# Performance work log

Measured on AMD Instinct MI355X. Metric: run time of the kernel, lower is better.

The kernel has to match this reference:

```python
import jax, jax.numpy as jnp
import numpy as np
import math

T, N, D = 512, 128, 64
H, HID, OUT = 4, 64, 64
BLOCK = 512


def setup_inputs() -> dict:
    key = jax.random.key(0)
    ks = jax.random.split(key, 6)
    x = jax.random.normal(ks[0], (T, N, D), dtype=jnp.float32)
    pe_table = jax.random.normal(ks[1], (BLOCK, N * D), dtype=jnp.float32) * 0.02
    wq = jax.random.normal(ks[2], (H, HID, D), dtype=jnp.float32) / math.sqrt(D)
    wk = jax.random.normal(ks[3], (H, HID, D), dtype=jnp.float32) / math.sqrt(D)
    wv = jax.random.normal(ks[4], (H, OUT, D), dtype=jnp.float32) / math.sqrt(D)
    wo = jax.random.normal(ks[5], (OUT, H * HID), dtype=jnp.float32) / math.sqrt(H * HID)
    return {"x": x, "pe_table": pe_table, "wq": wq, "wk": wk, "wv": wv, "wo": wo}


def reference(x, pe_table, wq, wk, wv, wo):
    # x: [T, N, D]. Positional encoding: embedding row per time index t.
    t, n, d = x.shape
    pe = pe_table[:t].reshape(t, n, d)
    xin = x + pe  # dropout is identity in eval mode

    hid = wq.shape[1]
    # nn.Linear(bias=False): y = x @ W.T, W is [out, in]
    Q = jnp.einsum('tnd,hed->htne', xin, wq)  # [H, T, N, HID]
    K = jnp.einsum('tnd,hed->htne', xin, wk)
    V = jnp.einsum('tnd,hod->htno', xin, wv)  # [H, T, N, OUT]

    # per-node attention over time: scores[h,t,n,s] = Q[h,t,n]·K[h,s,n] / sqrt(hid)
    scores = jnp.einsum('htne,hsne->htns', Q, K) / math.sqrt(hid)

    # causal (sequent) mask over (t, s), masked_fill(mask==0, -1e9)
    causal = jnp.tril(jnp.ones((t, t), dtype=bool))  # [T, T]
    scores = jnp.where(causal[None, :, None, :], scores, jnp.float32(-1e9))

    p = jax.nn.softmax(scores, axis=-1)  # [H, T, N, T]
    heads = jnp.einsum('htns,hsno->htno', p, V)  # [H, T, N, OUT]

    # concat heads along feature dim, then output projection
    heads = heads.transpose(1, 2, 0, 3).reshape(t, n, -1)  # [T, N, H*OUT]
    out = heads @ wo.T  # [T, N, OUT]
    return out
```

## Files before the change

kernel.cpp:

```cpp
#include <hip/hip_runtime.h>

using short8 = __attribute__((ext_vector_type(8))) short;
using f32x4  = __attribute__((ext_vector_type(4))) float;
using u16x4  = __attribute__((ext_vector_type(4))) unsigned short;

#define MFMA16(A,B,C) __builtin_amdgcn_mfma_f32_16x16x32_bf16((A),(B),(C),0,0,0)

#if __has_builtin(__builtin_amdgcn_exp2f)
#define EXP2(x) __builtin_amdgcn_exp2f(x)
#else
#define EXP2(x) exp2f(x)
#endif

__device__ __forceinline__ unsigned short f2b(float f) {
  unsigned u = __float_as_uint(f);
  return (unsigned short)((u + 0x7fffu + ((u >> 16) & 1u)) >> 16);
}
__device__ __forceinline__ short8 mk8(unsigned a, unsigned b, unsigned c, unsigned d) {
  union { unsigned u[4]; short8 s; } t; t.u[0]=a; t.u[1]=b; t.u[2]=c; t.u[3]=d; return t.s;
}
__device__ __forceinline__ unsigned pk2(float lo, float hi) {
  return __builtin_amdgcn_perm(__float_as_uint(hi), __float_as_uint(lo), 0x07060302u);
}


__global__ void prep_kernel(const float* __restrict__ x, const float* __restrict__ pe,
                            unsigned* __restrict__ xinT,
                            const float* __restrict__ wq, const float* __restrict__ wk,
                            const float* __restrict__ wv, const float* __restrict__ wo,
                            unsigned short* __restrict__ wP) {
  int b = blockIdx.x;
  if (b >= 8192) {
    int idx = (b - 8192) * 256 + threadIdx.x;
    int a = idx >> 14, e = idx & 16383;
    const float SC = 0.18033688011112042f;
    float v = (a == 0) ? wq[e] * SC : (a == 1) ? wk[e] : (a == 2) ? wv[e] : wo[e];
    wP[idx] = f2b(v);
    return;
  }
  int i2 = b * 256 + threadIdx.x;
  const float2* xp = (const float2*)x;
  const float2* pp = (const float2*)pe;
  float2 a = xp[i2], c = pp[i2];
  float s0 = a.x + c.x, s1 = a.y + c.y;
  int i = i2 << 1;
  int t = i >> 13, rem = i & 8191, n = rem >> 6, d = rem & 63;
  unsigned v = (unsigned)f2b(s0) | ((unsigned)f2b(s1) << 16);
  xinT[((n * 512 + t) * 64 + d) >> 1] = v;
}

__device__ __forceinline__ void qprojT(
    const unsigned short* xn, const unsigned short* bqP, int qb16,
    int lg, int lm, short8 (&qB)[2]) {
  const f32x4 zero4 = {0.f, 0.f, 0.f, 0.f};
  short8 aX0 = *(const short8*)(xn + (qb16 + lm) * 64 + lg * 8);
  short8 aX1 = *(const short8*)(xn + (qb16 + lm) * 64 + 32 + lg * 8);
  f32x4 qt[4];
#pragma unroll
  for (int nt = 0; nt < 4; ++nt) {
    const unsigned short* p = bqP + (nt * 16 + lm) * 64 + lg * 8;
    short8 w0 = *(const short8*)p;
    short8 w1 = *(const short8*)(p + 32);
    f32x4 a = zero4;
    a = MFMA16(w0, aX0, a);
    a = MFMA16(w1, aX1, a);
    qt[nt] = a;
  }
#pragma unroll
  for (int ks = 0; ks < 2; ++ks) {
    short8 q;
#pragma unroll
    for (int i = 0; i < 8; ++i) q[i] = (short)f2b(qt[2 * ks + (i >> 2)][i & 3]);
    qB[ks] = q;
  }
}

__device__ __forceinline__ void stage_slab(
    const unsigned short* xn, int slab, int lg, int lm, int l,
    const unsigned short* bkP, const unsigned short* bvP,
    unsigned short* sK, short8* sVf) {
  const f32x4 zero4 = {0.f, 0.f, 0.f, 0.f};
  int s0 = slab * 32;
  short8 aX[2][2];
#pragma unroll
  for (int km = 0; km < 2; ++km) {
    aX[km][0] = *(const short8*)(xn + (s0 + km * 16 + lm) * 64 + lg * 8);
    aX[km][1] = *(const short8*)(xn + (s0 + km * 16 + lm) * 64 + 32 + lg * 8);
  }
#pragma unroll
  for (int nt = 0; nt < 4; ++nt) {
    const unsigned short* bko = bkP + (nt * 16 + lm) * 64 + lg * 8;
    const unsigned short* bvo = bvP + (nt * 16 + lm) * 64 + lg * 8;
    short8 wk0 = *(const short8*)bko, wk1 = *(const short8*)(bko + 32);
    short8 wv0 = *(const short8*)bvo, wv1 = *(const short8*)(bvo + 32);
    f32x4 k0 = zero4, k1 = zero4, v0 = zero4, v1 = zero4;
    k0 = MFMA16(aX[0][0], wk0, k0); k0 = MFMA16(aX[0][1], wk1, k0);
    k1 = MFMA16(aX[1][0], wk0, k1); k1 = MFMA16(aX[1][1], wk1, k1);
    v0 = MFMA16(aX[0][0], wv0, v0); v0 = MFMA16(aX[0][1], wv1, v0);
    v1 = MFMA16(aX[1][0], wv0, v1); v1 = MFMA16(aX[1][1], wv1, v1);
    int pos = ((nt & 2) << 4) + ((lm >> 2) << 3) + ((nt & 1) << 2) + (lm & 3);
#pragma unroll
    for (int r = 0; r < 4; ++r) {
      int row0 = s0 + lg * 4 + r;
      int row1 = s0 + 16 + lg * 4 + r;
      sK[row0 * 64 + (pos ^ ((row0 & 7) << 3))] = f2b(k0[r]);
      sK[row1 * 64 + (pos ^ ((row1 & 7) << 3))] = f2b(k1[r]);
    }
    short8 vv;
    vv[0]=(short)f2b(v0[0]); vv[1]=(short)f2b(v0[1]);
    vv[2]=(short)f2b(v0[2]); vv[3]=(short)f2b(v0[3]);
    vv[4]=(short)f2b(v1[0]); vv[5]=(short)f2b(v1[1]);
    vv[6]=(short)f2b(v1[2]); vv[7]=(short)f2b(v1[3]);
    sVf[(slab * 4 + nt) * 64 + l] = vv;
  }
}

__device__ __forceinline__ void load_vB(const short8* sVf, int kb, int l, short8 (&vB)[4]) {
#pragma unroll
  for (int ot = 0; ot < 4; ++ot) vB[ot] = sVf[(((kb >> 5) * 4) + ot) * 64 + l];
}

__device__ __forceinline__ void slab_body(
    const unsigned short* sK, const short8 (&vB)[4], const short8 (&qB)[2][2],
    f32x4 (&oAcc)[2][4], f32x4 (&lsAcc)[2], const short8 ones,
    int qb, int kb, int lg, int lm) {
  const f32x4 zero4 = {0.f, 0.f, 0.f, 0.f};
  short8 aK[2][2];
#pragma unroll
  for (int km = 0; km < 2; ++km) {
    int row = kb + km * 16 + lm;
    int rb = row * 64, xorv = (row & 7) << 3;
    aK[km][0] = *(const short8*)&sK[rb + ((lg * 8) ^ xorv)];
    aK[km][1] = *(const short8*)&sK[rb + ((32 + lg * 8) ^ xorv)];
  }
  f32x4 st[2][2];
#pragma unroll
  for (int km = 0; km < 2; ++km)
#pragma unroll
    for (int qn = 0; qn < 2; ++qn) {
      f32x4 a = zero4;
      a = MFMA16(aK[km][0], qB[qn][0], a);
      a = MFMA16(aK[km][1], qB[qn][1], a);
      st[km][qn] = a;
    }
  if (kb == qb) {
#pragma unroll
    for (int km = 0; km < 2; ++km)
#pragma unroll
      for (int qn = 0; qn < 2; ++qn) {
        if (km == 0 && qn == 1) continue;
#pragma unroll
        for (int r = 0; r < 4; ++r) {
          int key = km * 16 + lg * 4 + r, qr = qn * 16 + lm;
          if (key > qr) st[km][qn][r] = -1e30f;
        }
      }
  }
#pragma unroll
  for (int km = 0; km < 2; ++km)
#pragma unroll
    for (int qn = 0; qn < 2; ++qn)
#pragma unroll
      for (int r = 0; r < 4; ++r) st[km][qn][r] = EXP2(st[km][qn][r]);
#pragma unroll
  for (int mo = 0; mo < 2; ++mo) {
    short8 pA = mk8(pk2(st[0][mo][0], st[0][mo][1]), pk2(st[0][mo][2], st[0][mo][3]),
                    pk2(st[1][mo][0], st[1][mo][1]), pk2(st[1][mo][2], st[1][mo][3]));
    lsAcc[mo] = MFMA16(ones, pA, lsAcc[mo]);
#pragma unroll
    for (int ot = 0; ot < 4; ++ot) oAcc[mo][ot] = MFMA16(vB[ot], pA, oAcc[mo][ot]);
  }
}

__global__ __launch_bounds__(512) void attn_kernel(
    const unsigned short* __restrict__ xinT,
    const unsigned short* __restrict__ wP,
    unsigned short* __restrict__ heads) {
  __shared__ unsigned short sK[512 * 64];
  __shared__ short8 sVf[16 * 4 * 64];

  const int hn = blockIdx.x;
  const int h  = hn & 3;
  const int n  = hn >> 2;
  const int w  = threadIdx.x >> 6;
  const int l  = threadIdx.x & 63;
  const int lg = l >> 4;
  const int lm = l & 15;

  const unsigned short* xn = xinT + n * (512 * 64);
  const f32x4 zero4 = {0.f, 0.f, 0.f, 0.f};
  const short8 ones = mk8(0x3F803F80u, 0x3F803F80u, 0x3F803F80u, 0x3F803F80u);

  const unsigned short* bqP = wP + h * 4096;
  const unsigned short* bkP = wP + 16384 + h * 4096;
  const unsigned short* bvP = wP + 32768 + h * 4096;

  stage_slab(xn, w * 2,     lg, lm, l, bkP, bvP, sK, sVf);
  stage_slab(xn, w * 2 + 1, lg, lm, l, bkP, bvP, sK, sVf);
  __syncthreads();

  for (int c = 0; c < 2; ++c) {
    const int chunk = c ? (15 - w) : w;
    const int qb = chunk * 32;

    short8 qB[2][2];
    qprojT(xn, bqP, qb,      lg, lm, qB[0]);
    qprojT(xn, bqP, qb + 16, lg, lm, qB[1]);

    f32x4 oAcc[2][4];
#pragma unroll
    for (int mo = 0; mo < 2; ++mo)
#pragma unroll
      for (int ot = 0; ot < 4; ++ot) oAcc[mo][ot] = zero4;
    f32x4 lsAcc[2] = {zero4, zero4};

    short8 vA[4], vBv[4];
    load_vB(sVf, 0, l, vA);
    int kb = 0;
    while (true) {
      if (kb + 32 <= qb) load_vB(sVf, kb + 32, l, vBv);
      slab_body(sK, vA, qB, oAcc, lsAcc, ones, qb, kb, lg, lm);
      if (kb >= qb) break;
      kb += 32;
      if (kb + 32 <= qb) load_vB(sVf, kb + 32, l, vA);
      slab_body(sK, vBv, qB, oAcc, lsAcc, ones, qb, kb, lg, lm);
      if (kb >= qb) break;
      kb += 32;
    }

#pragma unroll
    for (int mo = 0; mo < 2; ++mo) {
      float li = 1.0f / lsAcc[mo][0];
      unsigned short* base = heads + ((qb + mo * 16 + lm) * 128 + n) * 256 + h * 64 + lg * 4;
#pragma unroll
      for (int ot = 0; ot < 4; ++ot) {
        u16x4 v;
#pragma unroll
        for (int r = 0; r < 4; ++r) v[r] = f2b(oAcc[mo][ot][r] * li);
        *(u16x4*)(base + ot * 16) = v;
      }
    }
  }
}

__global__ __launch_bounds__(256) void outproj_kernel(
    const unsigned short* __restrict__ heads,
    const unsigned short* __restrict__ woP,
    float* __restrict__ out) {
  const int w  = threadIdx.x >> 6;
  const int l  = threadIdx.x & 63;
  const int lg = l >> 4, lm = l & 15;
  const f32x4 zero4 = {0.f, 0.f, 0.f, 0.f};

  short8 woB[4][8];
#pragma unroll
  for (int nt = 0; nt < 4; ++nt)
#pragma unroll
    for (int ks = 0; ks < 8; ++ks)
      woB[nt][ks] = *(const short8*)(woP + (nt * 16 + lm) * 256 + ks * 32 + lg * 8);

  const int wid = blockIdx.x * 4 + w;
  for (int it = 0; it < 2; ++it) {
    int r0 = (wid * 2 + it) * 16;
    f32x4 acc[4];
#pragma unroll
    for (int nt = 0; nt < 4; ++nt) acc[nt] = zero4;
#pragma unroll
    for (int ks = 0; ks < 8; ++ks) {
      short8 aF = *(const short8*)&heads[(r0 + lm) * 256 + ks * 32 + lg * 8];
#pragma unroll
      for (int nt = 0; nt < 4; ++nt)
        acc[nt] = MFMA16(aF, woB[nt][ks], acc[nt]);
    }
#pragma unroll
    for (int nt = 0; nt < 4; ++nt)
#pragma unroll
      for (int r = 0; r < 4; ++r)
        out[(r0 + lg * 4 + r) * 64 + nt * 16 + lm] = acc[nt][r];
  }
}

extern "C" void kernel_launch(void* const* d_in, const int* in_sizes, int n_in,
                              void* d_out, int out_size, void* d_ws, size_t ws_size,
                              hipStream_t stream) {
  const float* x  = (const float*)d_in[0];
  const float* pe = (const float*)d_in[1];
  const float* wq = (const float*)d_in[2];
  const float* wk = (const float*)d_in[3];
  const float* wv = (const float*)d_in[4];
  const float* wo = (const float*)d_in[5];

  unsigned short* xinT  = (unsigned short*)d_ws;
  unsigned short* heads = (unsigned short*)((char*)d_ws + (16u << 20));
  unsigned short* wPk   = (unsigned short*)((char*)d_ws + (48u << 20));

  prep_kernel<<<8448, 256, 0, stream>>>(x, pe, (unsigned*)xinT, wq, wk, wv, wo, wPk);
  attn_kernel<<<512, 512, 0, stream>>>(xinT, wPk, heads);
  outproj_kernel<<<512, 256, 0, stream>>>(heads, wPk + 49152, (float*)d_out);
}
```

Before: 68.49 us.

## Recompute V projection per key slab instead of staging V in shared memory

New measurement: 85.20 us. +24.4%, slower.

```diff
diff --git a/kernel.cpp b/kernel.cpp
--- a/kernel.cpp
+++ b/kernel.cpp
@@ -75,10 +75,9 @@
   }
 }
 
-__device__ __forceinline__ void stage_slab(
-    const unsigned short* xn, int slab, int lg, int lm, int l,
-    const unsigned short* bkP, const unsigned short* bvP,
-    unsigned short* sK, short8* sVf) {
+__device__ __forceinline__ void stage_kslab(
+    const unsigned short* xn, int slab, int lg, int lm,
+    const unsigned short* bkP, unsigned short* sK) {
   const f32x4 zero4 = {0.f, 0.f, 0.f, 0.f};
   int s0 = slab * 32;
   short8 aX[2][2];
@@ -90,14 +89,10 @@
 #pragma unroll
   for (int nt = 0; nt < 4; ++nt) {
     const unsigned short* bko = bkP + (nt * 16 + lm) * 64 + lg * 8;
-    const unsigned short* bvo = bvP + (nt * 16 + lm) * 64 + lg * 8;
     short8 wk0 = *(const short8*)bko, wk1 = *(const short8*)(bko + 32);
-    short8 wv0 = *(const short8*)bvo, wv1 = *(const short8*)(bvo + 32);
-    f32x4 k0 = zero4, k1 = zero4, v0 = zero4, v1 = zero4;
+    f32x4 k0 = zero4, k1 = zero4;
     k0 = MFMA16(aX[0][0], wk0, k0); k0 = MFMA16(aX[0][1], wk1, k0);
     k1 = MFMA16(aX[1][0], wk0, k1); k1 = MFMA16(aX[1][1], wk1, k1);
-    v0 = MFMA16(aX[0][0], wv0, v0); v0 = MFMA16(aX[0][1], wv1, v0);
-    v1 = MFMA16(aX[1][0], wv0, v1); v1 = MFMA16(aX[1][1], wv1, v1);
     int pos = ((nt & 2) << 4) + ((lm >> 2) << 3) + ((nt & 1) << 2) + (lm & 3);
 #pragma unroll
     for (int r = 0; r < 4; ++r) {
@@ -106,43 +101,51 @@
       sK[row0 * 64 + (pos ^ ((row0 & 7) << 3))] = f2b(k0[r]);
       sK[row1 * 64 + (pos ^ ((row1 & 7) << 3))] = f2b(k1[r]);
     }
+  }
+}
+
+__device__ __forceinline__ void slab_body(
+    const unsigned short* sK, const unsigned short* xn, const short8 (&wvB)[4][2],
+    const short8 (&qB)[2][2], f32x4 (&oAcc)[2][4], f32x4 (&lsAcc)[2],
+    const short8 ones, int qb, int kb, int lg, int lm) {
+  const f32x4 zero4 = {0.f, 0.f, 0.f, 0.f};
+  short8 xA[2][2];
+#pragma unroll
+  for (int km = 0; km < 2; ++km) {
+    xA[km][0] = *(const short8*)(xn + (kb + km * 16 + lm) * 64 + lg * 8);
+    xA[km][1] = *(const short8*)(xn + (kb + km * 16 + lm) * 64 + 32 + lg * 8);
+  }
+  short8 aK[2][2];
+#pragma unroll
+  for (int km = 0; km < 2; ++km) {
+    int row = kb + km * 16 + lm;
+    int rb = row * 64, xorv = (row & 7) << 3;
+    aK[km][0] = *(const short8*)&sK[rb + ((lg * 8) ^ xorv)];
+    aK[km][1] = *(const short8*)&sK[rb + ((32 + lg * 8) ^ xorv)];
+  }
+  f32x4 st[2][2];
+#pragma unroll
+  for (int km = 0; km < 2; ++km)
+#pragma unroll
+    for (int qn = 0; qn < 2; ++qn) {
+      f32x4 a = zero4;
+      a = MFMA16(aK[km][0], qB[qn][0], a);
+      a = MFMA16(aK[km][1], qB[qn][1], a);
+      st[km][qn] = a;
+    }
+  short8 vB[4];
+#pragma unroll
+  for (int nt = 0; nt < 4; ++nt) {
+    f32x4 v0 = zero4, v1 = zero4;
+    v0 = MFMA16(xA[0][0], wvB[nt][0], v0); v0 = MFMA16(xA[0][1], wvB[nt][1], v0);
+    v1 = MFMA16(xA[1][0], wvB[nt][0], v1); v1 = MFMA16(xA[1][1], wvB[nt][1], v1);
     short8 vv;
     vv[0]=(short)f2b(v0[0]); vv[1]=(short)f2b(v0[1]);
     vv[2]=(short)f2b(v0[2]); vv[3]=(short)f2b(v0[3]);
     vv[4]=(short)f2b(v1[0]); vv[5]=(short)f2b(v1[1]);
     vv[6]=(short)f2b(v1[2]); vv[7]=(short)f2b(v1[3]);
-    sVf[(slab * 4 + nt) * 64 + l] = vv;
-  }
-}
-
-__device__ __forceinline__ void load_vB(const short8* sVf, int kb, int l, short8 (&vB)[4]) {
-#pragma unroll
-  for (int ot = 0; ot < 4; ++ot) vB[ot] = sVf[(((kb >> 5) * 4) + ot) * 64 + l];
-}
-
-__device__ __forceinline__ void slab_body(
-    const unsigned short* sK, const short8 (&vB)[4], const short8 (&qB)[2][2],
-    f32x4 (&oAcc)[2][4], f32x4 (&lsAcc)[2], const short8 ones,
-    int qb, int kb, int lg, int lm) {
-  const f32x4 zero4 = {0.f, 0.f, 0.f, 0.f};
-  short8 aK[2][2];
-#pragma unroll
-  for (int km = 0; km < 2; ++km) {
-    int row = kb + km * 16 + lm;
-    int rb = row * 64, xorv = (row & 7) << 3;
-    aK[km][0] = *(const short8*)&sK[rb + ((lg * 8) ^ xorv)];
-    aK[km][1] = *(const short8*)&sK[rb + ((32 + lg * 8) ^ xorv)];
-  }
-  f32x4 st[2][2];
-#pragma unroll
-  for (int km = 0; km < 2; ++km)
-#pragma unroll
-    for (int qn = 0; qn < 2; ++qn) {
-      f32x4 a = zero4;
-      a = MFMA16(aK[km][0], qB[qn][0], a);
-      a = MFMA16(aK[km][1], qB[qn][1], a);
-      st[km][qn] = a;
-    }
+    vB[nt] = vv;
+  }
   if (kb == qb) {
 #pragma unroll
     for (int km = 0; km < 2; ++km)
@@ -177,7 +180,6 @@
     const unsigned short* __restrict__ wP,
     unsigned short* __restrict__ heads) {
   __shared__ unsigned short sK[512 * 64];
-  __shared__ short8 sVf[16 * 4 * 64];
 
   const int hn = blockIdx.x;
   const int h  = hn & 3;
@@ -195,8 +197,16 @@
   const unsigned short* bkP = wP + 16384 + h * 4096;
   const unsigned short* bvP = wP + 32768 + h * 4096;
 
-  stage_slab(xn, w * 2,     lg, lm, l, bkP, bvP, sK, sVf);
-  stage_slab(xn, w * 2 + 1, lg, lm, l, bkP, bvP, sK, sVf);
+  stage_kslab(xn, w * 2,     lg, lm, bkP, sK);
+  stage_kslab(xn, w * 2 + 1, lg, lm, bkP, sK);
+
+  short8 wvB[4][2];
+#pragma unroll
+  for (int nt = 0; nt < 4; ++nt)
+#pragma unroll
+    for (int ks = 0; ks < 2; ++ks)
+      wvB[nt][ks] = *(const short8*)(bvP + (nt * 16 + lm) * 64 + ks * 32 + lg * 8);
+
   __syncthreads();
 
   for (int c = 0; c < 2; ++c) {
@@ -214,19 +224,8 @@
       for (int ot = 0; ot < 4; ++ot) oAcc[mo][ot] = zero4;
     f32x4 lsAcc[2] = {zero4, zero4};
 
-    short8 vA[4], vBv[4];
-    load_vB(sVf, 0, l, vA);
-    int kb = 0;
-    while (true) {
-      if (kb + 32 <= qb) load_vB(sVf, kb + 32, l, vBv);
-      slab_body(sK, vA, qB, oAcc, lsAcc, ones, qb, kb, lg, lm);
-      if (kb >= qb) break;
-      kb += 32;
-      if (kb + 32 <= qb) load_vB(sVf, kb + 32, l, vA);
-      slab_body(sK, vBv, qB, oAcc, lsAcc, ones, qb, kb, lg, lm);
-      if (kb >= qb) break;
-      kb += 32;
-    }
+    for (int kb = 0; kb <= qb; kb += 32)
+      slab_body(sK, xn, wvB, qB, oAcc, lsAcc, ones, qb, kb, lg, lm);
 
 #pragma unroll
     for (int mo = 0; mo < 2; ++mo) {
```
